# Kernel optimization log

Measured on AMD Instinct MI355X. Metric: run time of the kernel, lower is better.

Reference implementation:

```python
import jax, jax.numpy as jnp
import numpy as np

WAY = 100; SHOT = 5; QUERY = 100; DIM = 2048; K_VALUE = 512
NQ = WAY * QUERY  # 10000 query samples


def _l2norm(x, axis=-1):
    n = jnp.linalg.norm(x, axis=axis, keepdims=True)
    return x / jnp.maximum(n, 1e-12)  # matches F.normalize eps


def _compute_logits(feat, proto, temp):
    # feat [1,Q,D], proto [1,W,D] -> [1,Q,W]; 'dot' metric
    logits = jnp.einsum('bqd,bwd->bqw', feat, proto)
    norm = jnp.linalg.norm(logits, axis=1, keepdims=True)  # L2 over query dim, [1,1,W]
    return logits / (norm + 1e-6) * temp


def _proto_refine(logits, feat, proto, k_value):
    # vectorized version of the original Python loop with .item() scatter-adds
    abs_cert = jnp.max(logits, axis=2)[0]                 # [Q]
    k = min(abs_cert.shape[0], k_value)
    vals, idxs = jax.lax.top_k(abs_cert, k)               # [k]
    pseudo = jnp.argmax(logits[0, idxs], axis=1)          # [k] pseudo labels
    wf = (vals[:, None] * feat[0, idxs]) / k              # [k,D]
    add = jnp.zeros(proto.shape[1:], feat.dtype).at[pseudo].add(wf)  # [W,D]
    return proto + add


def _distance(shot, feat, temp_proto, way):
    proto = _l2norm(jnp.mean(shot, axis=-2))  # [1,W,D]
    feat = _l2norm(feat)                      # [1,Q,D]
    logits = _compute_logits(feat, proto, temp_proto)
    proto = _proto_refine(logits, feat, proto, K_VALUE)
    logits = _compute_logits(feat, proto, temp_proto)
    return logits.reshape(-1, way)[None]      # [1,Q,W]


def _distill_loss(logits_l, logits_h, weight):
    # faithful to F.log_softmax/softmax over dim=1 (query dim) and the
    # per-batch-row weighted KL sum in the original
    logp = jax.nn.log_softmax(logits_l, axis=1)
    p = jax.nn.softmax(logits_h, axis=1)
    kl = p * (jnp.log(p) - logp)              # [B,Q,W]
    wT = weight.T                             # [Q,B]
    summed = jnp.stack([jnp.sum(kl[i] * wT[i]) for i in range(logits_l.shape[0])])
    return jnp.mean(summed) / (jnp.sum(weight) + 1e-8)


def _certainties(shot, query, temp_proto, way):
    pk = _distance(shot, query, temp_proto, way)
    abs_c = jnp.max(pk, axis=2)                           # [1,Q]
    p = jax.nn.softmax(pk, axis=-1)
    rel_c = jnp.sum(p * jnp.log(p + 1e-10), axis=2)       # [1,Q]
    return abs_c, rel_c


def setup_inputs() -> dict:
    key = jax.random.key(0)
    k1, k2, k3, k4 = jax.random.split(key, 4)
    return {
        'x_shot': jax.random.normal(k1, (1, WAY, SHOT, DIM), jnp.float32),
        'x_query': jax.random.normal(k2, (1, NQ, DIM), jnp.float32),
        'dct_shot': jax.random.normal(k3, (1, WAY, SHOT, DIM), jnp.float32),
        'dct_query': jax.random.normal(k4, (1, NQ, DIM), jnp.float32),
        'temp_proto': jnp.float32(10.0),
        'temp': jnp.float32(1.0),
        'temp_dct': jnp.float32(1.0),
    }


def reference(x_shot, x_query, dct_shot, dct_query, temp_proto, temp, temp_dct):
    way = x_shot.shape[1]
    abs_c, rel_c = _certainties(x_shot, x_query, temp_proto, way)
    abs_cd, rel_cd = _certainties(dct_shot, dct_query, temp_proto, way)
    diff = np.asarray(abs_c - abs_cd + rel_c - rel_cd)[0]
    res_idx = np.where(diff > 0)[0]
    dct_idx = np.where(diff < 0)[0]
    zero = jnp.float32(0.0)
    if res_idx.size == 0 and dct_idx.size == 0:
        loss_dctl = zero; loss_resl = zero
    elif res_idx.size != 0 and dct_idx.size == 0:
        lrh = _distance(x_shot, x_query, temp_proto, way)
        ldl = _distance(dct_shot, dct_query, temp_proto, way)
        loss_dctl = _distill_loss(ldl, lrh, abs_c); loss_resl = zero
    elif res_idx.size == 0:
        ldh = _distance(dct_shot, dct_query, temp_proto, way)
        lrl = _distance(x_shot, x_query, temp_proto, way)
        loss_resl = _distill_loss(lrl, ldh, abs_cd); loss_dctl = zero
    else:
        lrh = _distance(x_shot, x_query[:, res_idx], temp_proto, way)
        ldl = _distance(dct_shot, dct_query[:, res_idx], temp_proto, way)
        ldh = _distance(dct_shot, dct_query[:, dct_idx], temp_proto, way)
        lrl = _distance(x_shot, x_query[:, dct_idx], temp_proto, way)
        loss_dctl = _distill_loss(ldl, lrh, abs_c[:, res_idx])
        loss_resl = _distill_loss(lrl, ldh, abs_cd[:, dct_idx])
    denom = jnp.maximum(abs_c + abs_cd, 1e-8)
    w_r = (abs_c / denom).T  # [Q,1]
    w_f = (abs_cd / denom).T
    return (temp * loss_resl, temp_dct * loss_dctl,
            jnp.asarray(res_idx), jnp.asarray(dct_idx), w_r, w_f)
```

## Files before the change

kernel.cpp:

```cpp
#include <hip/hip_runtime.h>
#include <cstdint>
#include <cstddef>

#define WAYS  100
#define SHOTS 5
#define NQ    10000
#define DIM   2048
#define KSEL  512

#define BQ 128
#define BW 64
#define BK 32
#define PADQ 4
#define PADW 4
#define CQ 64

struct Ctrl {
  double klsum[2];
  double wsum[2];
  float  w0[2];
  int    R, Dn;
  unsigned int T[8];
  int rem[8];
  int kk[8];
};

__device__ __forceinline__ unsigned int monokey(float f){
  unsigned int b = __float_as_uint(f);
  return (b & 0x80000000u) ? ~b : (b | 0x80000000u);
}
__device__ __forceinline__ float dekey(unsigned int k){
  return (k & 0x80000000u) ? __uint_as_float(k & 0x7FFFFFFFu)
                           : __uint_as_float(~k);
}
__device__ __forceinline__ int decn(int sel, const Ctrl* c){
  return sel == 0 ? NQ : (sel == 1 ? c->R : c->Dn);
}

__global__ void proto_kernel(const float* __restrict__ xs, const float* __restrict__ dsh,
                             float* __restrict__ protoX, float* __restrict__ protoD){
  int b = blockIdx.x;
  const float* src = (b < WAYS) ? xs : dsh;
  float* dst = (b < WAYS) ? protoX : protoD;
  int w = (b < WAYS) ? b : b - WAYS;
  __shared__ float meanv[DIM];
  __shared__ float red[256];
  float loc = 0.f;
  for (int d = threadIdx.x; d < DIM; d += 256){
    float s = 0.f;
    for (int sh = 0; sh < SHOTS; sh++) s += src[((size_t)w*SHOTS + sh)*DIM + d];
    float m = s / (float)SHOTS;
    meanv[d] = m;
    loc += m*m;
  }
  red[threadIdx.x] = loc; __syncthreads();
  for (int st = 128; st > 0; st >>= 1){
    if (threadIdx.x < st) red[threadIdx.x] += red[threadIdx.x + st];
    __syncthreads();
  }
  float inv = 1.0f / fmaxf(sqrtf(red[0]), 1e-12f);
  for (int d = threadIdx.x; d < DIM; d += 256)
    dst[(size_t)w*DIM + d] = meanv[d] * inv;
}

__global__ __launch_bounds__(256)
void invnorm_kernel(const float* __restrict__ xq, const float* __restrict__ dq,
                    float* __restrict__ invnX, float* __restrict__ invnD){
  int row = blockIdx.x * 4 + (threadIdx.x >> 6);
  if (row >= 2*NQ) return;
  int lane = threadIdx.x & 63;
  const float* src = (row < NQ) ? xq : dq;
  float* dst = (row < NQ) ? invnX : invnD;
  int q = (row < NQ) ? row : row - NQ;
  const float4* r4 = (const float4*)(src + (size_t)q*DIM);
  float s = 0.f;
  for (int i = lane; i < DIM/4; i += 64){
    float4 v = r4[i];
    s += v.x*v.x + v.y*v.y + v.z*v.z + v.w*v.w;
  }
  for (int off = 32; off > 0; off >>= 1) s += __shfl_down(s, off);
  if (lane == 0) dst[q] = 1.0f / fmaxf(sqrtf(s), 1e-12f);
}

struct GemmArgs {
  const float* feat[4];
  const float* proto[4];
  const int*   idx[4];
  float*       outP[4];
  const float* invn[4];
  int          nSel[4];
  int          splitk;
  int          applyInvn;
  const Ctrl*  ctrl;
};

__global__ __launch_bounds__(256)
void gemm_batched(GemmArgs ga){
  int batch = blockIdx.z / ga.splitk;
  int s     = blockIdx.z % ga.splitk;
  int n = decn(ga.nSel[batch], ga.ctrl);
  int qBase = blockIdx.x * BQ;
  if (qBase >= n) return;
  int wBase = blockIdx.y * BW;
  int kLen  = DIM / ga.splitk;
  int kStart = s * kLen;

  __shared__ float As[BK][BQ+PADQ];
  __shared__ float Bs[BK][BW+PADW];

  const float* feat  = ga.feat[batch];
  const float* proto = ga.proto[batch];
  const int*   idxl  = ga.idx[batch];

  int tid = threadIdx.x;
  int qr = tid & 127;
  int arow = qBase + qr;
  int garow = idxl ? idxl[min(arow, n-1)] : min(arow, n-1);
  const float* pA = feat + (size_t)garow*DIM + kStart;
  int akk0 = tid >> 7;

  int wr = tid & 63;
  int gbrow = wBase + wr;
  bool bok = (gbrow < WAYS);
  const float* pB = proto + (size_t)gbrow*DIM + kStart;
  int bkk0 = tid >> 6;

  int tx = tid & 15;
  int ty = tid >> 4;
  float acc[8][4];
#pragma unroll
  for (int i = 0; i < 8; i++)
#pragma unroll
    for (int j = 0; j < 4; j++) acc[i][j] = 0.f;

  float4 av[4], bv[2];
#pragma unroll
  for (int i = 0; i < 4; i++) av[i] = *(const float4*)(pA + (akk0 + 2*i)*4);
#pragma unroll
  for (int i = 0; i < 2; i++)
    bv[i] = bok ? *(const float4*)(pB + (bkk0 + 4*i)*4) : make_float4(0.f,0.f,0.f,0.f);

  for (int k0 = 0; k0 < kLen; k0 += BK){
    __syncthreads();
#pragma unroll
    for (int i = 0; i < 4; i++){
      int kk = (akk0 + 2*i)*4;
      As[kk+0][qr] = av[i].x; As[kk+1][qr] = av[i].y;
      As[kk+2][qr] = av[i].z; As[kk+3][qr] = av[i].w;
    }
#pragma unroll
    for (int i = 0; i < 2; i++){
      int kk = (bkk0 + 4*i)*4;
      Bs[kk+0][wr] = bv[i].x; Bs[kk+1][wr] = bv[i].y;
      Bs[kk+2][wr] = bv[i].z; Bs[kk+3][wr] = bv[i].w;
    }
    __syncthreads();
    int k1 = k0 + BK;
    bool more = (k1 < kLen);
    if (more){
#pragma unroll
      for (int i = 0; i < 4; i++) av[i] = *(const float4*)(pA + k1 + (akk0 + 2*i)*4);
#pragma unroll
      for (int i = 0; i < 2; i++)
        bv[i] = bok ? *(const float4*)(pB + k1 + (bkk0 + 4*i)*4) : make_float4(0.f,0.f,0.f,0.f);
    }
#pragma unroll
    for (int kk2 = 0; kk2 < BK; kk2++){
      float4 a0 = *(const float4*)&As[kk2][ty*8];
      float4 a1 = *(const float4*)&As[kk2][ty*8+4];
      float4 b0 = *(const float4*)&Bs[kk2][tx*4];
      float a8[8] = {a0.x,a0.y,a0.z,a0.w,a1.x,a1.y,a1.z,a1.w};
      float b4[4] = {b0.x,b0.y,b0.z,b0.w};
#pragma unroll
      for (int i = 0; i < 8; i++)
#pragma unroll
        for (int j = 0; j < 4; j++)
          acc[i][j] += a8[i]*b4[j];
    }
  }
  float* outBase = ga.outP[batch] + (size_t)s*NQ*WAYS;
  int wc = wBase + tx*4;
#pragma unroll
  for (int i = 0; i < 8; i++){
    int q = qBase + ty*8 + i;
    if (q >= n) continue;
    float scr = 1.f;
    if (ga.applyInvn){
      int gq = idxl ? idxl[q] : q;
      scr = ga.invn[batch][gq];
    }
    float* dst = outBase + (size_t)q*WAYS + wc;
    if (wc + 3 < WAYS){
      *(float4*)dst = make_float4(acc[i][0]*scr, acc[i][1]*scr, acc[i][2]*scr, acc[i][3]*scr);
    } else {
#pragma unroll
      for (int j = 0; j < 4; j++) if (wc + j < WAYS) dst[j] = acc[i][j]*scr;
    }
  }
}

struct CombArgs {
  const float* P;
  const float* invn[2];
  float* Ltgt[2];
  double* colSq;
  int splitk;
};
__global__ __launch_bounds__(256)
void combine_batched(CombArgs ca){
  int b = blockIdx.y;
  int qBase = blockIdx.x * CQ;
  int t = threadIdx.x;
  int j = t % 25, r = t / 25;
  const float* Pb = ca.P + (size_t)b*ca.splitk*NQ*WAYS;
  const float* invn = ca.invn[b];
  float* L = ca.Ltgt[b];
  double sq0=0.0, sq1=0.0, sq2=0.0, sq3=0.0;
  if (r < 10){
    for (int i = r; i < CQ; i += 10){
      int q = qBase + i;
      if (q >= NQ) break;
      float sc = invn[q];
      const float* p0 = Pb + (size_t)q*WAYS + 4*j;
      float4 v = *(const float4*)p0;
      for (int s2 = 1; s2 < ca.splitk; s2++){
        float4 u = *(const float4*)(p0 + (size_t)s2*NQ*WAYS);
        v.x += u.x; v.y += u.y; v.z += u.z; v.w += u.w;
      }
      v.x *= sc; v.y *= sc; v.z *= sc; v.w *= sc;
      *(float4*)(L + (size_t)q*WAYS + 4*j) = v;
      sq0 += (double)v.x*(double)v.x;
      sq1 += (double)v.y*(double)v.y;
      sq2 += (double)v.z*(double)v.z;
      sq3 += (double)v.w*(double)v.w;
    }
  }
  __shared__ double red[WAYS][10];
  if (r < 10){
    red[4*j+0][r]=sq0; red[4*j+1][r]=sq1; red[4*j+2][r]=sq2; red[4*j+3][r]=sq3;
  }
  __syncthreads();
  if (t < WAYS){
    double s2 = 0.0;
#pragma unroll
    for (int rr = 0; rr < 10; rr++) s2 += red[t][rr];
    atomicAdd(ca.colSq + (size_t)b*WAYS + t, s2);
  }
}

struct StatArgs {
  const float* Lsrc[4];
  const int*   idx[4];
  int nSel[4];
  double* colSq;
  unsigned* maxK;
  unsigned* negK;
  const Ctrl* ctrl;
};
__global__ __launch_bounds__(256)
void stats_batched(StatArgs sa){
  int b = blockIdx.y;
  int n = decn(sa.nSel[b], sa.ctrl);
  int qBase = blockIdx.x * CQ;
  if (qBase >= n) return;
  int t = threadIdx.x;
  int j = t % 25, r = t / 25;
  double sq0=0.0, sq1=0.0, sq2=0.0, sq3=0.0;
  float mx0=-3.4e38f,mx1=-3.4e38f,mx2=-3.4e38f,mx3=-3.4e38f;
  float mn0= 3.4e38f,mn1= 3.4e38f,mn2= 3.4e38f,mn3= 3.4e38f;
  if (r < 10){
    const int* idx = sa.idx[b];
    const float* L = sa.Lsrc[b];
    for (int i = r; i < CQ; i += 10){
      int q = qBase + i;
      if (q >= n) break;
      int gq = idx ? idx[q] : q;
      float4 v = *(const float4*)(L + (size_t)gq*WAYS + 4*j);
      sq0 += (double)v.x*(double)v.x; sq1 += (double)v.y*(double)v.y;
      sq2 += (double)v.z*(double)v.z; sq3 += (double)v.w*(double)v.w;
      mx0=fmaxf(mx0,v.x); mx1=fmaxf(mx1,v.y); mx2=fmaxf(mx2,v.z); mx3=fmaxf(mx3,v.w);
      mn0=fminf(mn0,v.x); mn1=fminf(mn1,v.y); mn2=fminf(mn2,v.z); mn3=fminf(mn3,v.w);
    }
  }
  __shared__ double red[WAYS][10];
  if (r < 10){
    red[4*j+0][r]=sq0; red[4*j+1][r]=sq1; red[4*j+2][r]=sq2; red[4*j+3][r]=sq3;
  }
  __syncthreads();
  if (t < WAYS){
    double s2 = 0.0;
#pragma unroll
    for (int rr = 0; rr < 10; rr++) s2 += red[t][rr];
    atomicAdd(sa.colSq + (size_t)b*WAYS + t, s2);
  }
  if (sa.maxK){
    __shared__ float redMx[WAYS][10], redMn[WAYS][10];
    if (r < 10){
      redMx[4*j+0][r]=mx0; redMx[4*j+1][r]=mx1; redMx[4*j+2][r]=mx2; redMx[4*j+3][r]=mx3;
      redMn[4*j+0][r]=mn0; redMn[4*j+1][r]=mn1; redMn[4*j+2][r]=mn2; redMn[4*j+3][r]=mn3;
    }
    __syncthreads();
    if (t < WAYS){
      float mx = -3.4e38f, mn = 3.4e38f;
#pragma unroll
      for (int rr = 0; rr < 10; rr++){ mx = fmaxf(mx, redMx[t][rr]); mn = fminf(mn, redMn[t][rr]); }
      atomicMax(sa.maxK + (size_t)b*WAYS + t, monokey(mx));
      atomicMax(sa.negK + (size_t)b*WAYS + t, monokey(-mn));
    }
  }
}

struct RS1Args {
  const float* Lsrc[4];
  const int*   idx[4];
  int nSel[4];
  const double* colSq;
  const float* tpP;
  const Ctrl* ctrl;
  float* absCert; unsigned* keys; int* pseudo;
};
__global__ __launch_bounds__(256)
void rowstats1_b(RS1Args a){
  int b = blockIdx.y;
  int n = decn(a.nSel[b], a.ctrl);
  __shared__ float sc[WAYS];
  int t = threadIdx.x;
  if (t < WAYS) sc[t] = (*a.tpP) / ((float)sqrt(a.colSq[(size_t)b*WAYS+t]) + 1e-6f);
  __syncthreads();
  int q = blockIdx.x*256 + t;
  if (q >= n) return;
  int gq = a.idx[b] ? a.idx[b][q] : q;
  const float* row = a.Lsrc[b] + (size_t)gq*WAYS;
  float m = row[0]*sc[0]; int am = 0;
  for (int w = 1; w < WAYS; w++){
    float v = row[w]*sc[w];
    if (v > m){ m = v; am = w; }
  }
  a.absCert[(size_t)b*NQ+q] = m;
  a.pseudo [(size_t)b*NQ+q] = am;
  a.keys   [(size_t)b*NQ+q] = monokey(m);
}

struct RS2Args {
  const float* Lsrc[2];
  const double* colSq;
  const float* tpP;
  float* absC; float* relC;
};
__global__ __launch_bounds__(256)
void rowstats2_b(RS2Args a){
  int b = blockIdx.y;
  __shared__ float sc[WAYS];
  int t = threadIdx.x;
  if (t < WAYS) sc[t] = (*a.tpP) / ((float)sqrt(a.colSq[(size_t)b*WAYS+t]) + 1e-6f);
  __syncthreads();
  int q = blockIdx.x*256 + t;
  if (q >= NQ) return;
  const float* row = a.Lsrc[b] + (size_t)q*WAYS;
  float m = row[0]*sc[0];
  for (int w = 1; w < WAYS; w++) m = fmaxf(m, row[w]*sc[w]);
  float s = 0.f;
  for (int w = 0; w < WAYS; w++) s += expf(row[w]*sc[w] - m);
  float inv = 1.0f / s, rel = 0.f;
  for (int w = 0; w < WAYS; w++){
    float p = expf(row[w]*sc[w] - m) * inv;
    rel += p * logf(p + 1e-10f);
  }
  a.absC[(size_t)b*NQ+q] = m;
  a.relC[(size_t)b*NQ+q] = rel;
}

struct SGArgs {
  const unsigned* keys; const float* absCert;
  int nSel[4]; int instBase;
  int* selIdx; float* selVal;
  Ctrl* ctrl;
};
__global__ __launch_bounds__(1024)
void selectgather_b(SGArgs a){
  int b = blockIdx.x;
  int inst = a.instBase + b;
  int n = decn(a.nSel[b], a.ctrl);
  int k = n < KSEL ? n : KSEL;
  const unsigned* keys = a.keys + (size_t)b*NQ;
  const float* absCert = a.absCert + (size_t)b*NQ;
  int* selIdx = a.selIdx + b*KSEL;
  float* selVal = a.selVal + b*KSEL;
  __shared__ int hist[256];
  __shared__ unsigned sprefix;
  __shared__ int srem;
  int t = threadIdx.x;
  if (t == 0){ sprefix = 0u; srem = k; }
  __syncthreads();
  int nv4 = n >> 2;
  for (int pass = 0; pass < 4; pass++){
    int shift = 24 - 8*pass;
    if (t < 256) hist[t] = 0;
    __syncthreads();
    unsigned pref = sprefix;
    unsigned mask = (pass == 0) ? 0u : (0xFFFFFFFFu << (shift + 8));
    for (int i = t; i < nv4; i += 1024){
      uint4 kv = ((const uint4*)keys)[i];
      if ((kv.x & mask) == pref) atomicAdd(&hist[(kv.x >> shift) & 255], 1);
      if ((kv.y & mask) == pref) atomicAdd(&hist[(kv.y >> shift) & 255], 1);
      if ((kv.z & mask) == pref) atomicAdd(&hist[(kv.z >> shift) & 255], 1);
      if ((kv.w & mask) == pref) atomicAdd(&hist[(kv.w >> shift) & 255], 1);
    }
    for (int i = 4*nv4 + t; i < n; i += 1024){
      unsigned key = keys[i];
      if ((key & mask) == pref) atomicAdd(&hist[(key >> shift) & 255], 1);
    }
    __syncthreads();
    if (t == 0){
      int acc = 0, rem = srem, sel = 0;
      for (int b2 = 255; b2 >= 0; b2--){
        int h = hist[b2];
        if (acc + h >= rem){ sel = b2; srem = rem - acc; break; }
        acc += h;
      }
      sprefix = pref | ((unsigned)sel << shift);
    }
    __syncthreads();
  }
  unsigned T = sprefix;
  int rem = srem;
  if (t == 0){ a.ctrl->T[inst] = T; a.ctrl->rem[inst] = rem; a.ctrl->kk[inst] = k; }
  int cntGT = k - rem;
  const int CH = 10;
  int q0 = t*CH;
  int fg[CH], fe[CH]; int cg = 0, ce = 0;
  for (int i = 0; i < CH; i++){
    int q = q0 + i; int g = 0, e = 0;
    if (q < n){ unsigned key = keys[q]; g = key > T; e = (key == T); }
    fg[i] = g; fe[i] = e; cg += g; ce += e;
  }
  __shared__ int sG[1024], sE[1024];
  sG[t] = cg; sE[t] = ce; __syncthreads();
  for (int s = 1; s < 1024; s <<= 1){
    int vg = t >= s ? sG[t-s] : 0;
    int ve = t >= s ? sE[t-s] : 0;
    __syncthreads();
    sG[t] += vg; sE[t] += ve;
    __syncthreads();
  }
  int posG = sG[t] - cg, posE = sE[t] - ce;
  for (int i = 0; i < CH; i++){
    int q = q0 + i;
    if (q >= n) break;
    if (fg[i]){ selIdx[posG] = q; selVal[posG] = absCert[q]; posG++; }
    else if (fe[i]){
      if (posE < rem){ selIdx[cntGT+posE] = q; selVal[cntGT+posE] = absCert[q]; }
      posE++;
    }
  }
}

struct RefArgs {
  const float* feat[4]; const int* idx[4];
  const float* invn[4]; const float* proto[4];
  const int* selIdx; const float* selVal;
  const int* pseudo;
  float* protoRef;
  int instBase;
  const Ctrl* ctrl;
};
__global__ __launch_bounds__(256)
void refine_b(RefArgs a){
  int b = blockIdx.y;
  int w = blockIdx.x;
  int k = a.ctrl->kk[a.instBase + b];
  const int* selIdx = a.selIdx + b*KSEL;
  const float* selVal = a.selVal + b*KSEL;
  const int* pseudo = a.pseudo + (size_t)b*NQ;
  const int* idxl = a.idx[b];
  __shared__ int   sRow[KSEL];
  __shared__ float sCoef[KSEL];
  int t = threadIdx.x;
  for (int j = t; j < k; j += 256){
    int srow = selIdx[j];
    int grow = idxl ? idxl[srow] : srow;
    sRow[j]  = (pseudo[srow] == w) ? grow : -1;
    sCoef[j] = selVal[j] * a.invn[b][grow] / (float)k;
  }
  __syncthreads();
  float4 acc0 = make_float4(0.f,0.f,0.f,0.f);
  float4 acc1 = make_float4(0.f,0.f,0.f,0.f);
  int d0 = t*4, d1 = t*4 + 1024;
  const float* feat = a.feat[b];
  for (int j = 0; j < k; j++){
    int grow = sRow[j];
    if (grow < 0) continue;
    float c = sCoef[j];
    const float* fr = feat + (size_t)grow*DIM;
    float4 f0 = *(const float4*)(fr + d0);
    float4 f1 = *(const float4*)(fr + d1);
    acc0.x += c*f0.x; acc0.y += c*f0.y; acc0.z += c*f0.z; acc0.w += c*f0.w;
    acc1.x += c*f1.x; acc1.y += c*f1.y; acc1.z += c*f1.z; acc1.w += c*f1.w;
  }
  const float* pw = a.proto[b] + (size_t)w*DIM;
  float* pr = a.protoRef + ((size_t)b*WAYS + w)*DIM;
  float4 p0 = *(const float4*)(pw + d0);
  float4 p1 = *(const float4*)(pw + d1);
  *(float4*)(pr + d0) = make_float4(p0.x+acc0.x, p0.y+acc0.y, p0.z+acc0.z, p0.w+acc0.w);
  *(float4*)(pr + d1) = make_float4(p1.x+acc1.x, p1.y+acc1.y, p1.z+acc1.z, p1.w+acc1.w);
}

__global__ __launch_bounds__(1024)
void diff_partition(const float* __restrict__ absC, const float* __restrict__ relC,
                    Ctrl* ctrl, int* __restrict__ resIdx, int* __restrict__ dctIdx,
                    float* __restrict__ out){
  const float* absCx = absC;        const float* absCd = absC + NQ;
  const float* relCx = relC;        const float* relCd = relC + NQ;
  const int CH = 10;
  int t = threadIdx.x, q0 = t*CH;
  int fr[CH], fd[CH]; int cr = 0, cd = 0;
  for (int i = 0; i < CH; i++){
    int q = q0 + i; int r = 0, dn = 0;
    if (q < NQ){
      float dv = absCx[q] - absCd[q] + relCx[q] - relCd[q];
      r = dv > 0.f; dn = dv < 0.f;
    }
    fr[i] = r; fd[i] = dn; cr += r; cd += dn;
  }
  __shared__ int sR[1024], sD[1024];
  sR[t] = cr; sD[t] = cd; __syncthreads();
  for (int s = 1; s < 1024; s <<= 1){
    int vr = t >= s ? sR[t-s] : 0;
    int vd = t >= s ? sD[t-s] : 0;
    __syncthreads();
    sR[t] += vr; sD[t] += vd;
    __syncthreads();
  }
  int R = sR[1023], Dn = sD[1023];
  int posR = sR[t] - cr, posD = sD[t] - cd;
  if (t == 0){ ctrl->R = R; ctrl->Dn = Dn; }
  for (int i = 0; i < CH; i++){
    int q = q0 + i;
    if (q >= NQ) break;
    if (fr[i]){ resIdx[posR] = q; out[2+posR] = (float)q; posR++; }
    if (fd[i]){ dctIdx[posD] = q; out[2+R+posD] = (float)q; posD++; }
  }
  for (int q = t; q < NQ; q += 1024){
    float a = absCx[q], b = absCd[q];
    float den = fmaxf(a + b, 1e-8f);
    out[2+R+Dn+q]      = a / den;
    out[2+R+Dn+NQ+q]   = b / den;
  }
}

struct SEArgs {
  const float* Lsrc[4];
  int nSel[4];
  const double* colSq;
  const unsigned* maxK; const unsigned* negK;
  double* sumExp;
  const float* tpP;
  const Ctrl* ctrl;
};
__global__ __launch_bounds__(256)
void sumexp_batched(SEArgs a){
  int b = blockIdx.y;
  int n = decn(a.nSel[b], a.ctrl);
  int t = threadIdx.x;
  __shared__ float sc[WAYS], mv[WAYS];
  if (t < WAYS){
    float s = (*a.tpP) / ((float)sqrt(a.colSq[(size_t)b*WAYS+t]) + 1e-6f);
    float mxv = dekey(a.maxK[(size_t)b*WAYS+t]);
    float mnv = -dekey(a.negK[(size_t)b*WAYS+t]);
    sc[t] = s; mv[t] = (s >= 0.f) ? s*mxv : s*mnv;
  }
  __syncthreads();
  int qBase = blockIdx.x * CQ;
  if (qBase >= n) return;
  int j = t % 25, r = t / 25;
  double e0=0.0,e1=0.0,e2=0.0,e3=0.0;
  if (r < 10){
    const float* L = a.Lsrc[b];
    float s0=sc[4*j+0], s1=sc[4*j+1], s2=sc[4*j+2], s3=sc[4*j+3];
    float m0=mv[4*j+0], m1=mv[4*j+1], m2=mv[4*j+2], m3=mv[4*j+3];
    for (int i = r; i < CQ; i += 10){
      int q = qBase + i;
      if (q >= n) break;
      float4 v = *(const float4*)(L + (size_t)q*WAYS + 4*j);
      e0 += (double)expf(v.x*s0 - m0);
      e1 += (double)expf(v.y*s1 - m1);
      e2 += (double)expf(v.z*s2 - m2);
      e3 += (double)expf(v.w*s3 - m3);
    }
  }
  __shared__ double red[WAYS][10];
  if (r < 10){
    red[4*j+0][r]=e0; red[4*j+1][r]=e1; red[4*j+2][r]=e2; red[4*j+3][r]=e3;
  }
  __syncthreads();
  if (t < WAYS){
    double s2 = 0.0;
#pragma unroll
    for (int rr = 0; rr < 10; rr++) s2 += red[t][rr];
    atomicAdd(a.sumExp + (size_t)b*WAYS + t, s2);
  }
}

struct KLArgs {
  const float* bufs[4];
  const double* colSq2;
  const unsigned* maxK; const unsigned* negK; const double* sumExp;
  const float* tpP;
  Ctrl* ctrl;
};
__global__ __launch_bounds__(256)
void klsum_batched(KLArgs a){
  int p = blockIdx.y;
  int bL = p ? 3 : 1, bH = p ? 2 : 0;
  int n = p ? a.ctrl->Dn : a.ctrl->R;
  __shared__ float scL[WAYS], lseL[WAYS], scH[WAYS], lseH[WAYS];
  int t = threadIdx.x;
  if (t < WAYS){
    float tp = *a.tpP;
    {
      float s = tp / ((float)sqrt(a.colSq2[(size_t)bL*WAYS+t]) + 1e-6f);
      float mxv = dekey(a.maxK[(size_t)bL*WAYS+t]);
      float mnv = -dekey(a.negK[(size_t)bL*WAYS+t]);
      float m = (s >= 0.f) ? s*mxv : s*mnv;
      scL[t] = s; lseL[t] = m + (float)log(a.sumExp[(size_t)bL*WAYS+t]);
    }
    {
      float s = tp / ((float)sqrt(a.colSq2[(size_t)bH*WAYS+t]) + 1e-6f);
      float mxv = dekey(a.maxK[(size_t)bH*WAYS+t]);
      float mnv = -dekey(a.negK[(size_t)bH*WAYS+t]);
      float m = (s >= 0.f) ? s*mxv : s*mnv;
      scH[t] = s; lseH[t] = m + (float)log(a.sumExp[(size_t)bH*WAYS+t]);
    }
  }
  __syncthreads();
  const float* Lm = a.bufs[bL];
  const float* Hm = a.bufs[bH];
  size_t total = (size_t)n * WAYS;
  double loc = 0.0;
  for (size_t i = (size_t)blockIdx.x*256 + t; i < total; i += (size_t)gridDim.x*256){
    int w = (int)(i % WAYS);
    float lh = Hm[i]*scH[w] - lseH[w];
    float ll = Lm[i]*scL[w] - lseL[w];
    loc += (double)(expf(lh) * (lh - ll));
  }
  __shared__ double sd[256];
  sd[t] = loc; __syncthreads();
  for (int st = 128; st > 0; st >>= 1){
    if (t < st) sd[t] += sd[t + st];
    __syncthreads();
  }
  if (t == 0) atomicAdd(&a.ctrl->klsum[p], sd[0]);
}

__global__ __launch_bounds__(256)
void wsum_b(const float* __restrict__ absC, const int* __restrict__ resIdx,
            const int* __restrict__ dctIdx, Ctrl* ctrl){
  int b = blockIdx.y;
  int n = b ? ctrl->Dn : ctrl->R;
  const float* src = b ? (absC + NQ) : absC;
  const int* idx = b ? dctIdx : resIdx;
  double loc = 0.0;
  for (int i = blockIdx.x*256 + threadIdx.x; i < n; i += gridDim.x*256)
    loc += (double)src[idx[i]];
  __shared__ double sd[256];
  sd[threadIdx.x] = loc; __syncthreads();
  for (int st = 128; st > 0; st >>= 1){
    if (threadIdx.x < st) sd[threadIdx.x] += sd[threadIdx.x + st];
    __syncthreads();
  }
  if (threadIdx.x == 0) atomicAdd(&ctrl->wsum[b], sd[0]);
  if (blockIdx.x == 0 && threadIdx.x == 0 && n > 0) ctrl->w0[b] = src[idx[0]];
}

__global__ void final_kernel(const Ctrl* ctrl, const float* tP, const float* tdP,
                             float* out){
  if (threadIdx.x == 0 && blockIdx.x == 0){
    float lossd = ctrl->w0[0] * (float)ctrl->klsum[0] / ((float)ctrl->wsum[0] + 1e-8f);
    float lossr = ctrl->w0[1] * (float)ctrl->klsum[1] / ((float)ctrl->wsum[1] + 1e-8f);
    out[0] = (*tP)  * lossr;
    out[1] = (*tdP) * lossd;
  }
}

extern "C" void kernel_launch(void* const* d_in, const int* in_sizes, int n_in,
                              void* d_out, int out_size, void* d_ws, size_t ws_size,
                              hipStream_t stream)
{
  const float* xs  = (const float*)d_in[0];
  const float* xq  = (const float*)d_in[1];
  const float* dsh = (const float*)d_in[2];
  const float* dq  = (const float*)d_in[3];
  const float* tpP = (const float*)d_in[4];
  const float* tP  = (const float*)d_in[5];
  const float* tdP = (const float*)d_in[6];
  float* out = (float*)d_out;

  char* base = (char*)d_ws;
  Ctrl* ctrl = (Ctrl*)base;
  double*   colSqAll = (double*)(base + 512);
  unsigned* maxK     = (unsigned*)(base + 512 + 9600);
  unsigned* negK     = maxK + 4*WAYS;
  double*   sumExp   = (double*)(base + 512 + 9600 + 3200);
  size_t zone = 512 + 9600 + 3200 + 3200;
  size_t off = (zone + 255) & ~(size_t)255;
  auto alloc = [&](size_t nElem)->void*{ void* p = base + off; off += nElem*4; return p; };
  float* protoX   = (float*)alloc((size_t)WAYS*DIM);
  float* protoD   = (float*)alloc((size_t)WAYS*DIM);
  float* protoRef = (float*)alloc((size_t)6*WAYS*DIM);
  float* invnX    = (float*)alloc(NQ);
  float* invnD    = (float*)alloc(NQ);
  float* Lx0      = (float*)alloc((size_t)NQ*WAYS);
  float* Ld0      = (float*)alloc((size_t)NQ*WAYS);
  float* bufs     = (float*)alloc((size_t)4*NQ*WAYS);
  float* absCertF = (float*)alloc((size_t)2*NQ);
  unsigned* keysF = (unsigned*)alloc((size_t)2*NQ);
  int*   pseudoF  = (int*)alloc((size_t)2*NQ);
  float* absCertS = (float*)alloc((size_t)4*NQ);
  unsigned* keysS = (unsigned*)alloc((size_t)4*NQ);
  int*   pseudoS  = (int*)alloc((size_t)4*NQ);
  float* absC     = (float*)alloc((size_t)2*NQ);
  float* relC     = (float*)alloc((size_t)2*NQ);
  int*   selIdx   = (int*)alloc((size_t)4*KSEL);
  float* selVal   = (float*)alloc((size_t)4*KSEL);
  int*   resIdx   = (int*)alloc(NQ);
  int*   dctIdx   = (int*)alloc(NQ);
  if (off > ws_size) return;
  float* LxF = bufs;
  float* LdF = bufs + (size_t)NQ*WAYS;

  float* P = (float*)(base + off);
  int splitkF;
  if      (off + (size_t)8*NQ*WAYS*4 <= ws_size) splitkF = 4;
  else if (off + (size_t)4*NQ*WAYS*4 <= ws_size) splitkF = 2;
  else splitkF = 1;

  hipMemsetAsync(base, 0, zone, stream);
  proto_kernel<<<2*WAYS, 256, 0, stream>>>(xs, dsh, protoX, protoD);
  invnorm_kernel<<<(2*NQ+3)/4, 256, 0, stream>>>(xq, dq, invnX, invnD);

  dim3 gFull(( NQ + BQ - 1)/BQ, (WAYS + BW - 1)/BW, 2*splitkF);
  int sgrid = (NQ + CQ - 1)/CQ;

  GemmArgs g1{};
  g1.feat[0]=xq; g1.feat[1]=dq;
  g1.proto[0]=protoX; g1.proto[1]=protoD;
  g1.nSel[0]=0; g1.nSel[1]=0;
  g1.splitk=splitkF; g1.ctrl=ctrl;
  if (splitkF > 1){
    g1.outP[0]=P; g1.outP[1]=P + (size_t)splitkF*NQ*WAYS; g1.applyInvn=0;
  } else {
    g1.outP[0]=Lx0; g1.outP[1]=Ld0; g1.applyInvn=1;
    g1.invn[0]=invnX; g1.invn[1]=invnD;
  }
  gemm_batched<<<gFull,256,0,stream>>>(g1);
  if (splitkF > 1){
    CombArgs c1{}; c1.P=P; c1.invn[0]=invnX; c1.invn[1]=invnD;
    c1.Ltgt[0]=Lx0; c1.Ltgt[1]=Ld0; c1.colSq=colSqAll; c1.splitk=splitkF;
    combine_batched<<<dim3(sgrid,2),256,0,stream>>>(c1);
  } else {
    StatArgs s1{}; s1.Lsrc[0]=Lx0; s1.Lsrc[1]=Ld0;
    s1.nSel[0]=0; s1.nSel[1]=0; s1.colSq=colSqAll; s1.ctrl=ctrl;
    stats_batched<<<dim3(sgrid,2),256,0,stream>>>(s1);
  }
  RS1Args r1{}; r1.Lsrc[0]=Lx0; r1.Lsrc[1]=Ld0;
  r1.nSel[0]=0; r1.nSel[1]=0; r1.colSq=colSqAll; r1.tpP=tpP; r1.ctrl=ctrl;
  r1.absCert=absCertF; r1.keys=keysF; r1.pseudo=pseudoF;
  rowstats1_b<<<dim3((NQ+255)/256,2),256,0,stream>>>(r1);
  SGArgs sg1{}; sg1.keys=keysF; sg1.absCert=absCertF;
  sg1.nSel[0]=0; sg1.nSel[1]=0; sg1.instBase=0;
  sg1.selIdx=selIdx; sg1.selVal=selVal; sg1.ctrl=ctrl;
  selectgather_b<<<2,1024,0,stream>>>(sg1);
  RefArgs rf1{}; rf1.feat[0]=xq; rf1.feat[1]=dq;
  rf1.invn[0]=invnX; rf1.invn[1]=invnD;
  rf1.proto[0]=protoX; rf1.proto[1]=protoD;
  rf1.selIdx=selIdx; rf1.selVal=selVal; rf1.pseudo=pseudoF;
  rf1.protoRef=protoRef; rf1.instBase=0; rf1.ctrl=ctrl;
  refine_b<<<dim3(WAYS,2),256,0,stream>>>(rf1);

  GemmArgs g2 = g1;
  g2.proto[0]=protoRef; g2.proto[1]=protoRef + (size_t)WAYS*DIM;
  if (splitkF == 1){ g2.outP[0]=LxF; g2.outP[1]=LdF; }
  gemm_batched<<<gFull,256,0,stream>>>(g2);
  if (splitkF > 1){
    CombArgs c2{}; c2.P=P; c2.invn[0]=invnX; c2.invn[1]=invnD;
    c2.Ltgt[0]=LxF; c2.Ltgt[1]=LdF; c2.colSq=colSqAll + 2*WAYS; c2.splitk=splitkF;
    combine_batched<<<dim3(sgrid,2),256,0,stream>>>(c2);
  } else {
    StatArgs s2{}; s2.Lsrc[0]=LxF; s2.Lsrc[1]=LdF;
    s2.nSel[0]=0; s2.nSel[1]=0; s2.colSq=colSqAll + 2*WAYS; s2.ctrl=ctrl;
    stats_batched<<<dim3(sgrid,2),256,0,stream>>>(s2);
  }
  RS2Args r2{}; r2.Lsrc[0]=LxF; r2.Lsrc[1]=LdF;
  r2.colSq=colSqAll + 2*WAYS; r2.tpP=tpP; r2.absC=absC; r2.relC=relC;
  rowstats2_b<<<dim3((NQ+255)/256,2),256,0,stream>>>(r2);

  diff_partition<<<1,1024,0,stream>>>(absC, relC, ctrl, resIdx, dctIdx, out);

  StatArgs ss1{};
  ss1.Lsrc[0]=Lx0; ss1.Lsrc[1]=Ld0; ss1.Lsrc[2]=Ld0; ss1.Lsrc[3]=Lx0;
  ss1.idx[0]=resIdx; ss1.idx[1]=resIdx; ss1.idx[2]=dctIdx; ss1.idx[3]=dctIdx;
  ss1.nSel[0]=1; ss1.nSel[1]=1; ss1.nSel[2]=2; ss1.nSel[3]=2;
  ss1.colSq=colSqAll + 4*WAYS; ss1.ctrl=ctrl;
  stats_batched<<<dim3(sgrid,4),256,0,stream>>>(ss1);
  RS1Args rs{}; rs.Lsrc[0]=Lx0; rs.Lsrc[1]=Ld0; rs.Lsrc[2]=Ld0; rs.Lsrc[3]=Lx0;
  rs.idx[0]=resIdx; rs.idx[1]=resIdx; rs.idx[2]=dctIdx; rs.idx[3]=dctIdx;
  rs.nSel[0]=1; rs.nSel[1]=1; rs.nSel[2]=2; rs.nSel[3]=2;
  rs.colSq=colSqAll + 4*WAYS; rs.tpP=tpP; rs.ctrl=ctrl;
  rs.absCert=absCertS; rs.keys=keysS; rs.pseudo=pseudoS;
  rowstats1_b<<<dim3((NQ+255)/256,4),256,0,stream>>>(rs);
  SGArgs sg2{}; sg2.keys=keysS; sg2.absCert=absCertS;
  sg2.nSel[0]=1; sg2.nSel[1]=1; sg2.nSel[2]=2; sg2.nSel[3]=2; sg2.instBase=2;
  sg2.selIdx=selIdx; sg2.selVal=selVal; sg2.ctrl=ctrl;
  selectgather_b<<<4,1024,0,stream>>>(sg2);
  RefArgs rf2{};
  rf2.feat[0]=xq; rf2.feat[1]=dq; rf2.feat[2]=dq; rf2.feat[3]=xq;
  rf2.idx[0]=resIdx; rf2.idx[1]=resIdx; rf2.idx[2]=dctIdx; rf2.idx[3]=dctIdx;
  rf2.invn[0]=invnX; rf2.invn[1]=invnD; rf2.invn[2]=invnD; rf2.invn[3]=invnX;
  rf2.proto[0]=protoX; rf2.proto[1]=protoD; rf2.proto[2]=protoD; rf2.proto[3]=protoX;
  rf2.selIdx=selIdx; rf2.selVal=selVal; rf2.pseudo=pseudoS;
  rf2.protoRef=protoRef + (size_t)2*WAYS*DIM; rf2.instBase=2; rf2.ctrl=ctrl;
  refine_b<<<dim3(WAYS,4),256,0,stream>>>(rf2);
  GemmArgs gs{};
  gs.feat[0]=xq; gs.feat[1]=dq; gs.feat[2]=dq; gs.feat[3]=xq;
  for (int b = 0; b < 4; b++){
    gs.proto[b] = protoRef + (size_t)(2+b)*WAYS*DIM;
    gs.outP[b]  = bufs + (size_t)b*NQ*WAYS;
  }
  gs.idx[0]=resIdx; gs.idx[1]=resIdx; gs.idx[2]=dctIdx; gs.idx[3]=dctIdx;
  gs.invn[0]=invnX; gs.invn[1]=invnD; gs.invn[2]=invnD; gs.invn[3]=invnX;
  gs.nSel[0]=1; gs.nSel[1]=1; gs.nSel[2]=2; gs.nSel[3]=2;
  gs.splitk=1; gs.applyInvn=1; gs.ctrl=ctrl;
  gemm_batched<<<dim3((NQ+BQ-1)/BQ,(WAYS+BW-1)/BW,4),256,0,stream>>>(gs);
  StatArgs ss2{};
  for (int b = 0; b < 4; b++) ss2.Lsrc[b] = bufs + (size_t)b*NQ*WAYS;
  ss2.nSel[0]=1; ss2.nSel[1]=1; ss2.nSel[2]=2; ss2.nSel[3]=2;
  ss2.colSq=colSqAll + 8*WAYS; ss2.maxK=maxK; ss2.negK=negK; ss2.ctrl=ctrl;
  stats_batched<<<dim3(sgrid,4),256,0,stream>>>(ss2);
  SEArgs se{};
  for (int b = 0; b < 4; b++) se.Lsrc[b] = bufs + (size_t)b*NQ*WAYS;
  se.nSel[0]=1; se.nSel[1]=1; se.nSel[2]=2; se.nSel[3]=2;
  se.colSq=colSqAll + 8*WAYS; se.maxK=maxK; se.negK=negK;
  se.sumExp=sumExp; se.tpP=tpP; se.ctrl=ctrl;
  sumexp_batched<<<dim3(sgrid,4),256,0,stream>>>(se);
  KLArgs kl{};
  for (int b = 0; b < 4; b++) kl.bufs[b] = bufs + (size_t)b*NQ*WAYS;
  kl.colSq2=colSqAll + 8*WAYS; kl.maxK=maxK; kl.negK=negK; kl.sumExp=sumExp;
  kl.tpP=tpP; kl.ctrl=ctrl;
  klsum_batched<<<dim3(64,2),256,0,stream>>>(kl);
  wsum_b<<<dim3((NQ+255)/256,2),256,0,stream>>>(absC, resIdx, dctIdx, ctrl);
  final_kernel<<<1,64,0,stream>>>(ctrl, tP, tdP, out);
}
```

Baseline: 1.028 ms.

## Shrink GEMM tile, cap split-K at two, and pack stage-2 logits into shared buffers

Halves the GEMM query tile from 128 to 64 rows with a 4x4 per-thread micro-tile, giving more blocks for the small-N stage. Caps split-K at 2 instead of 4. Drops the separate 4-batch logits buffer: the stage-2 batches now write into the split-K partial buffers, with the dct-selected rows placed after the first R rows through a new row-offset field read by the stats, sumexp and KL kernels. This cuts workspace size and memory traffic, but each thread does less work per shared-memory load and the full-size first GEMM gets less split-K parallelism.

```diff
diff --git a/kernel.cpp b/kernel.cpp
--- a/kernel.cpp
+++ b/kernel.cpp
@@ -8,11 +8,10 @@
 #define DIM   2048
 #define KSEL  512
 
-#define BQ 128
+#define BQ 64
 #define BW 64
 #define BK 32
-#define PADQ 4
-#define PADW 4
+#define PAD 4
 #define CQ 64
 
 struct Ctrl {
@@ -89,6 +88,7 @@
   float*       outP[4];
   const float* invn[4];
   int          nSel[4];
+  int          offSel[4];
   int          splitk;
   int          applyInvn;
   const Ctrl*  ctrl;
@@ -105,84 +105,68 @@
   int kLen  = DIM / ga.splitk;
   int kStart = s * kLen;
 
-  __shared__ float As[BK][BQ+PADQ];
-  __shared__ float Bs[BK][BW+PADW];
+  __shared__ float As[BK][BQ+PAD];
+  __shared__ float Bs[BK][BW+PAD];
 
   const float* feat  = ga.feat[batch];
   const float* proto = ga.proto[batch];
   const int*   idxl  = ga.idx[batch];
 
-  int tid = threadIdx.x;
-  int qr = tid & 127;
-  int arow = qBase + qr;
+  int t = threadIdx.x;
+  int lr = t & 63;
+  int kv = t >> 6;
+  int arow = qBase + lr;
   int garow = idxl ? idxl[min(arow, n-1)] : min(arow, n-1);
-  const float* pA = feat + (size_t)garow*DIM + kStart;
-  int akk0 = tid >> 7;
-
-  int wr = tid & 63;
-  int gbrow = wBase + wr;
-  bool bok = (gbrow < WAYS);
-  const float* pB = proto + (size_t)gbrow*DIM + kStart;
-  int bkk0 = tid >> 6;
-
-  int tx = tid & 15;
-  int ty = tid >> 4;
-  float acc[8][4];
+  const float* pA = feat + (size_t)garow*DIM + kStart + kv*4;
+  int wrow = wBase + lr;
+  bool bok = (wrow < WAYS);
+  const float* pB = proto + (size_t)wrow*DIM + kStart + kv*4;
+
+  int tx = t & 15, ty = t >> 4;
+  float acc[4][4];
 #pragma unroll
-  for (int i = 0; i < 8; i++)
+  for (int i = 0; i < 4; i++)
 #pragma unroll
     for (int j = 0; j < 4; j++) acc[i][j] = 0.f;
 
-  float4 av[4], bv[2];
-#pragma unroll
-  for (int i = 0; i < 4; i++) av[i] = *(const float4*)(pA + (akk0 + 2*i)*4);
-#pragma unroll
-  for (int i = 0; i < 2; i++)
-    bv[i] = bok ? *(const float4*)(pB + (bkk0 + 4*i)*4) : make_float4(0.f,0.f,0.f,0.f);
+  float4 av0, av1, bv0, bv1;
+  const float4 z4 = make_float4(0.f,0.f,0.f,0.f);
+  av0 = *(const float4*)pA;
+  av1 = *(const float4*)(pA + 16);
+  bv0 = bok ? *(const float4*)pB : z4;
+  bv1 = bok ? *(const float4*)(pB + 16) : z4;
 
   for (int k0 = 0; k0 < kLen; k0 += BK){
     __syncthreads();
-#pragma unroll
-    for (int i = 0; i < 4; i++){
-      int kk = (akk0 + 2*i)*4;
-      As[kk+0][qr] = av[i].x; As[kk+1][qr] = av[i].y;
-      As[kk+2][qr] = av[i].z; As[kk+3][qr] = av[i].w;
-    }
-#pragma unroll
-    for (int i = 0; i < 2; i++){
-      int kk = (bkk0 + 4*i)*4;
-      Bs[kk+0][wr] = bv[i].x; Bs[kk+1][wr] = bv[i].y;
-      Bs[kk+2][wr] = bv[i].z; Bs[kk+3][wr] = bv[i].w;
-    }
-    __syncthreads();
-    int k1 = k0 + BK;
-    bool more = (k1 < kLen);
-    if (more){
-#pragma unroll
-      for (int i = 0; i < 4; i++) av[i] = *(const float4*)(pA + k1 + (akk0 + 2*i)*4);
-#pragma unroll
-      for (int i = 0; i < 2; i++)
-        bv[i] = bok ? *(const float4*)(pB + k1 + (bkk0 + 4*i)*4) : make_float4(0.f,0.f,0.f,0.f);
+    int kk = kv*4;
+    As[kk+0 ][lr]=av0.x; As[kk+1 ][lr]=av0.y; As[kk+2 ][lr]=av0.z; As[kk+3 ][lr]=av0.w;
+    As[kk+16][lr]=av1.x; As[kk+17][lr]=av1.y; As[kk+18][lr]=av1.z; As[kk+19][lr]=av1.w;
+    Bs[kk+0 ][lr]=bv0.x; Bs[kk+1 ][lr]=bv0.y; Bs[kk+2 ][lr]=bv0.z; Bs[kk+3 ][lr]=bv0.w;
+    Bs[kk+16][lr]=bv1.x; Bs[kk+17][lr]=bv1.y; Bs[kk+18][lr]=bv1.z; Bs[kk+19][lr]=bv1.w;
+    __syncthreads();
+    if (k0 + BK < kLen){
+      const float* qA = pA + k0 + BK;
+      const float* qB = pB + k0 + BK;
+      av0 = *(const float4*)qA; av1 = *(const float4*)(qA + 16);
+      bv0 = bok ? *(const float4*)qB : z4;
+      bv1 = bok ? *(const float4*)(qB + 16) : z4;
     }
 #pragma unroll
     for (int kk2 = 0; kk2 < BK; kk2++){
-      float4 a0 = *(const float4*)&As[kk2][ty*8];
-      float4 a1 = *(const float4*)&As[kk2][ty*8+4];
-      float4 b0 = *(const float4*)&Bs[kk2][tx*4];
-      float a8[8] = {a0.x,a0.y,a0.z,a0.w,a1.x,a1.y,a1.z,a1.w};
-      float b4[4] = {b0.x,b0.y,b0.z,b0.w};
-#pragma unroll
-      for (int i = 0; i < 8; i++)
-#pragma unroll
-        for (int j = 0; j < 4; j++)
-          acc[i][j] += a8[i]*b4[j];
-    }
-  }
-  float* outBase = ga.outP[batch] + (size_t)s*NQ*WAYS;
+      float4 a = *(const float4*)&As[kk2][ty*4];
+      float4 b = *(const float4*)&Bs[kk2][tx*4];
+      acc[0][0]+=a.x*b.x; acc[0][1]+=a.x*b.y; acc[0][2]+=a.x*b.z; acc[0][3]+=a.x*b.w;
+      acc[1][0]+=a.y*b.x; acc[1][1]+=a.y*b.y; acc[1][2]+=a.y*b.z; acc[1][3]+=a.y*b.w;
+      acc[2][0]+=a.z*b.x; acc[2][1]+=a.z*b.y; acc[2][2]+=a.z*b.z; acc[2][3]+=a.z*b.w;
+      acc[3][0]+=a.w*b.x; acc[3][1]+=a.w*b.y; acc[3][2]+=a.w*b.z; acc[3][3]+=a.w*b.w;
+    }
+  }
+  int rowOff = ga.offSel[batch] ? ga.ctrl->R : 0;
+  float* outBase = ga.outP[batch] + ((size_t)s*NQ + (size_t)rowOff)*WAYS;
   int wc = wBase + tx*4;
 #pragma unroll
-  for (int i = 0; i < 8; i++){
-    int q = qBase + ty*8 + i;
+  for (int i = 0; i < 4; i++){
+    int q = qBase + ty*4 + i;
     if (q >= n) continue;
     float scr = 1.f;
     if (ga.applyInvn){
@@ -252,6 +236,7 @@
   const float* Lsrc[4];
   const int*   idx[4];
   int nSel[4];
+  int offSel[4];
   double* colSq;
   unsigned* maxK;
   unsigned* negK;
@@ -270,7 +255,8 @@
   float mn0= 3.4e38f,mn1= 3.4e38f,mn2= 3.4e38f,mn3= 3.4e38f;
   if (r < 10){
     const int* idx = sa.idx[b];
-    const float* L = sa.Lsrc[b];
+    int rowOff = sa.offSel[b] ? sa.ctrl->R : 0;
+    const float* L = sa.Lsrc[b] + (size_t)rowOff*WAYS;
     for (int i = r; i < CQ; i += 10){
       int q = qBase + i;
       if (q >= n) break;
@@ -551,6 +537,7 @@
 struct SEArgs {
   const float* Lsrc[4];
   int nSel[4];
+  int offSel[4];
   const double* colSq;
   const unsigned* maxK; const unsigned* negK;
   double* sumExp;
@@ -575,7 +562,8 @@
   int j = t % 25, r = t / 25;
   double e0=0.0,e1=0.0,e2=0.0,e3=0.0;
   if (r < 10){
-    const float* L = a.Lsrc[b];
+    int rowOff = a.offSel[b] ? a.ctrl->R : 0;
+    const float* L = a.Lsrc[b] + (size_t)rowOff*WAYS;
     float s0=sc[4*j+0], s1=sc[4*j+1], s2=sc[4*j+2], s3=sc[4*j+3];
     float m0=mv[4*j+0], m1=mv[4*j+1], m2=mv[4*j+2], m3=mv[4*j+3];
     for (int i = r; i < CQ; i += 10){
@@ -603,6 +591,7 @@
 
 struct KLArgs {
   const float* bufs[4];
+  int offSel[4];
   const double* colSq2;
   const unsigned* maxK; const unsigned* negK; const double* sumExp;
   const float* tpP;
@@ -633,8 +622,8 @@
     }
   }
   __syncthreads();
-  const float* Lm = a.bufs[bL];
-  const float* Hm = a.bufs[bH];
+  const float* Lm = a.bufs[bL] + (size_t)(a.offSel[bL] ? a.ctrl->R : 0)*WAYS;
+  const float* Hm = a.bufs[bH] + (size_t)(a.offSel[bH] ? a.ctrl->R : 0)*WAYS;
   size_t total = (size_t)n * WAYS;
   double loc = 0.0;
   for (size_t i = (size_t)blockIdx.x*256 + t; i < total; i += (size_t)gridDim.x*256){
@@ -706,12 +695,11 @@
   auto alloc = [&](size_t nElem)->void*{ void* p = base + off; off += nElem*4; return p; };
   float* protoX   = (float*)alloc((size_t)WAYS*DIM);
   float* protoD   = (float*)alloc((size_t)WAYS*DIM);
-  float* protoRef = (float*)alloc((size_t)6*WAYS*DIM);
+  float* protoRef = (float*)alloc((size_t)4*WAYS*DIM);
   float* invnX    = (float*)alloc(NQ);
   float* invnD    = (float*)alloc(NQ);
   float* Lx0      = (float*)alloc((size_t)NQ*WAYS);
   float* Ld0      = (float*)alloc((size_t)NQ*WAYS);
-  float* bufs     = (float*)alloc((size_t)4*NQ*WAYS);
   float* absCertF = (float*)alloc((size_t)2*NQ);
   unsigned* keysF = (unsigned*)alloc((size_t)2*NQ);
   int*   pseudoF  = (int*)alloc((size_t)2*NQ);
@@ -724,21 +712,23 @@
   float* selVal   = (float*)alloc((size_t)4*KSEL);
   int*   resIdx   = (int*)alloc(NQ);
   int*   dctIdx   = (int*)alloc(NQ);
-  if (off > ws_size) return;
-  float* LxF = bufs;
-  float* LdF = bufs + (size_t)NQ*WAYS;
-
-  float* P = (float*)(base + off);
+
+  float* P = (float*)(base + ((off + 255) & ~(size_t)255));
+  size_t offP = (off + 255) & ~(size_t)255;
   int splitkF;
-  if      (off + (size_t)8*NQ*WAYS*4 <= ws_size) splitkF = 4;
-  else if (off + (size_t)4*NQ*WAYS*4 <= ws_size) splitkF = 2;
-  else splitkF = 1;
+  if (offP + (size_t)2*2*NQ*WAYS*4 <= ws_size) splitkF = 2;
+  else if (offP + (size_t)2*1*NQ*WAYS*4 <= ws_size) splitkF = 1;
+  else return;
+  float* Pb0 = P;
+  float* Pb1 = P + (size_t)splitkF*NQ*WAYS;
+  float* LxF = Pb0;
+  float* LdF = Pb1;
 
   hipMemsetAsync(base, 0, zone, stream);
   proto_kernel<<<2*WAYS, 256, 0, stream>>>(xs, dsh, protoX, protoD);
   invnorm_kernel<<<(2*NQ+3)/4, 256, 0, stream>>>(xq, dq, invnX, invnD);
 
-  dim3 gFull(( NQ + BQ - 1)/BQ, (WAYS + BW - 1)/BW, 2*splitkF);
+  dim3 gFull((NQ + BQ - 1)/BQ, (WAYS + BW - 1)/BW, 2*splitkF);
   int sgrid = (NQ + CQ - 1)/CQ;
 
   GemmArgs g1{};
@@ -747,7 +737,7 @@
   g1.nSel[0]=0; g1.nSel[1]=0;
   g1.splitk=splitkF; g1.ctrl=ctrl;
   if (splitkF > 1){
-    g1.outP[0]=P; g1.outP[1]=P + (size_t)splitkF*NQ*WAYS; g1.applyInvn=0;
+    g1.outP[0]=Pb0; g1.outP[1]=Pb1; g1.applyInvn=0;
   } else {
     g1.outP[0]=Lx0; g1.outP[1]=Ld0; g1.applyInvn=1;
     g1.invn[0]=invnX; g1.invn[1]=invnD;
@@ -818,32 +808,37 @@
   rf2.invn[0]=invnX; rf2.invn[1]=invnD; rf2.invn[2]=invnD; rf2.invn[3]=invnX;
   rf2.proto[0]=protoX; rf2.proto[1]=protoD; rf2.proto[2]=protoD; rf2.proto[3]=protoX;
   rf2.selIdx=selIdx; rf2.selVal=selVal; rf2.pseudo=pseudoS;
-  rf2.protoRef=protoRef + (size_t)2*WAYS*DIM; rf2.instBase=2; rf2.ctrl=ctrl;
+  rf2.protoRef=protoRef; rf2.instBase=2; rf2.ctrl=ctrl;
   refine_b<<<dim3(WAYS,4),256,0,stream>>>(rf2);
   GemmArgs gs{};
   gs.feat[0]=xq; gs.feat[1]=dq; gs.feat[2]=dq; gs.feat[3]=xq;
-  for (int b = 0; b < 4; b++){
-    gs.proto[b] = protoRef + (size_t)(2+b)*WAYS*DIM;
-    gs.outP[b]  = bufs + (size_t)b*NQ*WAYS;
-  }
+  gs.proto[0]=protoRef;
+  gs.proto[1]=protoRef + (size_t)WAYS*DIM;
+  gs.proto[2]=protoRef + (size_t)2*WAYS*DIM;
+  gs.proto[3]=protoRef + (size_t)3*WAYS*DIM;
+  gs.outP[0]=Pb0; gs.outP[1]=Pb1; gs.outP[2]=Pb1; gs.outP[3]=Pb0;
+  gs.offSel[0]=0; gs.offSel[1]=0; gs.offSel[2]=1; gs.offSel[3]=1;
   gs.idx[0]=resIdx; gs.idx[1]=resIdx; gs.idx[2]=dctIdx; gs.idx[3]=dctIdx;
   gs.invn[0]=invnX; gs.invn[1]=invnD; gs.invn[2]=invnD; gs.invn[3]=invnX;
   gs.nSel[0]=1; gs.nSel[1]=1; gs.nSel[2]=2; gs.nSel[3]=2;
   gs.splitk=1; gs.applyInvn=1; gs.ctrl=ctrl;
   gemm_batched<<<dim3((NQ+BQ-1)/BQ,(WAYS+BW-1)/BW,4),256,0,stream>>>(gs);
   StatArgs ss2{};
-  for (int b = 0; b < 4; b++) ss2.Lsrc[b] = bufs + (size_t)b*NQ*WAYS;
+  ss2.Lsrc[0]=Pb0; ss2.Lsrc[1]=Pb1; ss2.Lsrc[2]=Pb1; ss2.Lsrc[3]=Pb0;
+  ss2.offSel[0]=0; ss2.offSel[1]=0; ss2.offSel[2]=1; ss2.offSel[3]=1;
   ss2.nSel[0]=1; ss2.nSel[1]=1; ss2.nSel[2]=2; ss2.nSel[3]=2;
   ss2.colSq=colSqAll + 8*WAYS; ss2.maxK=maxK; ss2.negK=negK; ss2.ctrl=ctrl;
   stats_batched<<<dim3(sgrid,4),256,0,stream>>>(ss2);
   SEArgs se{};
-  for (int b = 0; b < 4; b++) se.Lsrc[b] = bufs + (size_t)b*NQ*WAYS;
+  se.Lsrc[0]=Pb0; se.Lsrc[1]=Pb1; se.Lsrc[2]=Pb1; se.Lsrc[3]=Pb0;
+  se.offSel[0]=0; se.offSel[1]=0; se.offSel[2]=1; se.offSel[3]=1;
   se.nSel[0]=1; se.nSel[1]=1; se.nSel[2]=2; se.nSel[3]=2;
   se.colSq=colSqAll + 8*WAYS; se.maxK=maxK; se.negK=negK;
   se.sumExp=sumExp; se.tpP=tpP; se.ctrl=ctrl;
   sumexp_batched<<<dim3(sgrid,4),256,0,stream>>>(se);
   KLArgs kl{};
-  for (int b = 0; b < 4; b++) kl.bufs[b] = bufs + (size_t)b*NQ*WAYS;
+  kl.bufs[0]=Pb0; kl.bufs[1]=Pb1; kl.bufs[2]=Pb1; kl.bufs[3]=Pb0;
+  kl.offSel[0]=0; kl.offSel[1]=0; kl.offSel[2]=1; kl.offSel[3]=1;
   kl.colSq2=colSqAll + 8*WAYS; kl.maxK=maxK; kl.negK=negK; kl.sumExp=sumExp;
   kl.tpP=tpP; kl.ctrl=ctrl;
   klsum_batched<<<dim3(64,2),256,0,stream>>>(kl);
```

New measurement: 1.106 ms. 1.08x slower.
